# Kernel optimization log

Measured on AMD Instinct MI355X. Metric: run time of the kernel, lower is better.

## Reference

```python
import jax, jax.numpy as jnp
import numpy as np

EPS = 1e-3  # keras BatchNormalization default epsilon
K = 16


def _graph_feature(x, k):
    # x: [B, N, C] -> edge: [B, N, k, 2C]
    sq = jnp.sum(x * x, axis=-1)                       # [B, N]
    # negative squared distance (larger = closer); self is max
    pd = 2.0 * jnp.einsum('bnc,bmc->bnm', x, x) - sq[:, :, None] - sq[:, None, :]
    _, idx = jax.lax.top_k(pd, k)                      # [B, N, k]
    nbr = jax.vmap(lambda xb, ib: xb[ib])(x, idx)      # [B, N, k, C]
    ctr = jnp.broadcast_to(x[:, :, None, :], nbr.shape)
    return jnp.concatenate([ctr, nbr], axis=-1)        # [B, N, k, 2C]


def _bn(y, g, b, m, v):
    return (y - m) * (g * jax.lax.rsqrt(v + EPS)) + b


def _edge_block(x, W, g, b, m, v, k):
    e = _graph_feature(x, k)                           # [B, N, k, 2C]
    h = jnp.einsum('bnkc,cd->bnkd', e, W)              # 1x1 conv, no bias
    h = jax.nn.relu(_bn(h, g, b, m, v))
    return jnp.max(h, axis=2)                          # [B, N, D]


def setup_inputs() -> dict:
    key = jax.random.key(0)
    ks = jax.random.split(key, 32)
    B, N = 8, 2048
    x = jax.random.normal(ks[0], (B, N, 3), dtype=jnp.float32)
    dims = [(6, 64), (128, 64), (128, 128), (256, 256), (512, 512)]
    d = {'x': x}
    for i, (cin, cout) in enumerate(dims):
        j = i + 1
        d[f'W{j}'] = jax.random.normal(ks[1 + i], (cin, cout), dtype=jnp.float32) * (1.0 / np.sqrt(cin))
        d[f'g{j}'] = jax.random.uniform(ks[6 + i], (cout,), dtype=jnp.float32, minval=0.5, maxval=1.5)
        d[f'b{j}'] = jax.random.normal(ks[11 + i], (cout,), dtype=jnp.float32) * 0.1
        d[f'm{j}'] = jax.random.normal(ks[16 + i], (cout,), dtype=jnp.float32) * 0.1
        d[f'v{j}'] = jax.random.uniform(ks[21 + i], (cout,), dtype=jnp.float32, minval=0.5, maxval=1.5)
    return d


def reference(x, W1, g1, b1, m1, v1, W2, g2, b2, m2, v2, W3, g3, b3, m3, v3,
              W4, g4, b4, m4, v4, W5, g5, b5, m5, v5):
    x1 = _edge_block(x,  W1, g1, b1, m1, v1, K)   # [B, N, 64]
    x2 = _edge_block(x1, W2, g2, b2, m2, v2, K)   # [B, N, 64]
    x3 = _edge_block(x2, W3, g3, b3, m3, v3, K)   # [B, N, 128]
    x4 = _edge_block(x3, W4, g4, b4, m4, v4, K)   # [B, N, 256]
    x5 = jnp.concatenate([x1, x2, x3, x4], axis=-1)  # [B, N, 512]
    h5 = jnp.einsum('bnc,cd->bnd', x5, W5)           # 1x1 conv1d, no bias
    return jax.nn.relu(_bn(h5, g5, b5, m5, v5))      # [B, N, 512]
```

## Files before the change

kernel.cpp:

```cpp
#include <hip/hip_runtime.h>

#define NP 2048
#define BTOT 8
#define BN_TOT 16384
#define KC 16
#define NTILE 32
#define NEG_INF (-__builtin_inff())

typedef __attribute__((ext_vector_type(8))) short short8;
typedef __attribute__((ext_vector_type(4))) float f32x4;

__device__ __forceinline__ unsigned short bf16_rne(float x) {
  unsigned u = __float_as_uint(x);
  u += 0x7FFFu + ((u >> 16) & 1u);
  return (unsigned short)(u >> 16);
}
__device__ __forceinline__ void split2(float x, unsigned short& h, unsigned short& l) {
  h = bf16_rne(x);
  float hf = __uint_as_float((unsigned)h << 16);
  l = bf16_rne(x - hf);
}

__global__ __launch_bounds__(256) void dist_gemm(const float* __restrict__ X, int lda, int K,
                                                 const float* __restrict__ sq,
                                                 float* __restrict__ pd, int batch0) {
  int bz = blockIdx.z;
  const float* Xb = X + (size_t)(batch0 + bz) * NP * lda;
  const float* sqb = sq + (size_t)(batch0 + bz) * NP;
  float* pdb = pd + (size_t)bz * NP * NP;
  int rem = blockIdx.x, bi = 0;
  while (rem >= NTILE - bi) { rem -= NTILE - bi; ++bi; }
  int bj = bi + rem;
  int i0 = bi * 64, j0 = bj * 64;
  __shared__ float At[KC][68];
  __shared__ float Bt[KC][68];
  int t = threadIdx.x;
  int tx = t & 15, ty = t >> 4;
  int lk = t & 15, lr = t >> 4;
  float acc[4][4] = {};
  for (int k0 = 0; k0 < K; k0 += KC) {
    int kk = k0 + lk;
    bool kv = kk < K;
#pragma unroll
    for (int u = 0; u < 4; ++u) {
      int r = lr + u * 16;
      At[lk][r] = kv ? Xb[(size_t)(i0 + r) * lda + kk] : 0.f;
      Bt[lk][r] = kv ? Xb[(size_t)(j0 + r) * lda + kk] : 0.f;
    }
    __syncthreads();
#pragma unroll
    for (int q = 0; q < KC; ++q) {
      float4 a4 = *(const float4*)&At[q][ty * 4];
      float4 b4 = *(const float4*)&Bt[q][tx * 4];
      float a[4] = {a4.x, a4.y, a4.z, a4.w};
      float bv[4] = {b4.x, b4.y, b4.z, b4.w};
#pragma unroll
      for (int ii = 0; ii < 4; ++ii)
#pragma unroll
        for (int jj = 0; jj < 4; ++jj)
          acc[ii][jj] = fmaf(a[ii], bv[jj], acc[ii][jj]);
    }
    __syncthreads();
  }
  float4 sqj4 = *(const float4*)&sqb[j0 + tx * 4];
#pragma unroll
  for (int ii = 0; ii < 4; ++ii) {
    int i = i0 + ty * 4 + ii;
    float4 o;
    o.x = 2.f * acc[ii][0] - sqj4.x;
    o.y = 2.f * acc[ii][1] - sqj4.y;
    o.z = 2.f * acc[ii][2] - sqj4.z;
    o.w = 2.f * acc[ii][3] - sqj4.w;
    *(float4*)&pdb[(size_t)i * NP + j0 + tx * 4] = o;
  }
  if (bi != bj) {
    float4 sqi4 = *(const float4*)&sqb[i0 + ty * 4];
#pragma unroll
    for (int jj = 0; jj < 4; ++jj) {
      int j = j0 + tx * 4 + jj;
      float4 o;
      o.x = 2.f * acc[0][jj] - sqi4.x;
      o.y = 2.f * acc[1][jj] - sqi4.y;
      o.z = 2.f * acc[2][jj] - sqi4.z;
      o.w = 2.f * acc[3][jj] - sqi4.w;
      *(float4*)&pdb[(size_t)j * NP + i0 + ty * 4] = o;
    }
  }
}

template <typename JM>
__device__ __forceinline__ void select16(const float (&v)[32], int lane, float* svw,
                                         int* sjw, int* out, int jb, JM jmap) {
  float lmax = v[0];
#pragma unroll
  for (int t = 1; t < 32; ++t) lmax = fmaxf(lmax, v[t]);
  int rank = 0;
  for (int s = 0; s < 64; ++s) {
    float o = __shfl(lmax, s, 64);
    rank += (o > lmax) || (o == lmax && s < lane);
  }
  unsigned long long m15 = __ballot(rank == 15);
  float T0 = __shfl(lmax, (int)__builtin_ctzll(m15), 64);

  unsigned long long lowmask = (1ull << lane) - 1ull;
  unsigned keepmask = 0u;
  int base = 0;
#pragma unroll
  for (int t = 0; t < 32; ++t) {
    bool keep = (v[t] >= T0);
    unsigned long long mk = __ballot(keep);
    if (keep) {
      keepmask |= (1u << t);
      int pos = base + (int)__popcll(mk & lowmask);
      if (pos < 256) { svw[pos] = v[t]; sjw[pos] = jmap(t); }
    }
    base += (int)__popcll(mk);
  }
  int cnt = base;

  if (cnt <= 64) {
    __threadfence_block();
    float mv = NEG_INF;
    int mj = 1 << 30;
    if (lane < cnt) { mv = svw[lane]; mj = sjw[lane]; }
    int rk = 0;
    for (int s = 0; s < 64; ++s) {
      float ov = __shfl(mv, s, 64);
      int oj = __shfl(mj, s, 64);
      rk += (ov > mv) || (ov == mv && oj < mj);
    }
    if (lane < cnt && rk < 16) out[rk] = jb + mj;
    return;
  }

  if (cnt <= 256) {
    __threadfence_block();
    for (int r = 0; r < 16; ++r) {
      float lbv = NEG_INF;
      int lbj = 1 << 30, lbp = -1;
      for (int i = lane; i < cnt; i += 64) {
        float cv = svw[i];
        int cj = sjw[i];
        if (cv > lbv || (cv == lbv && cj < lbj)) { lbv = cv; lbj = cj; lbp = i; }
      }
      float bv = lbv;
      int bj = lbj;
#pragma unroll
      for (int off = 32; off > 0; off >>= 1) {
        float ov = __shfl_xor(bv, off, 64);
        int oj = __shfl_xor(bj, off, 64);
        if (ov > bv || (ov == bv && oj < bj)) { bv = ov; bj = oj; }
      }
      if (lane == 0) out[r] = jb + bj;
      if (lbp >= 0 && lbj == bj) svw[lbp] = NEG_INF;
      __threadfence_block();
    }
    return;
  }

  {
    unsigned avail = keepmask;
    for (int r = 0; r < 16; ++r) {
      float bv = NEG_INF;
      int bj = 1 << 30, bt = -1;
      unsigned am = avail;
      while (am) {
        int t = __builtin_ctz(am);
        am &= am - 1;
        float vv = v[t];
        int jj = jmap(t);
        if (vv > bv || (vv == bv && jj < bj)) { bv = vv; bj = jj; bt = t; }
      }
      float gv = bv;
      int gj = bj;
#pragma unroll
      for (int off = 32; off > 0; off >>= 1) {
        float ov = __shfl_xor(gv, off, 64);
        int oj = __shfl_xor(gj, off, 64);
        if (ov > gv || (ov == gv && oj < gj)) { gv = ov; gj = oj; }
      }
      if (lane == 0) out[r] = jb + gj;
      if (bt >= 0 && bj == gj) avail &= ~(1u << bt);
    }
  }
}

__global__ __launch_bounds__(256) void topk_kernel(const float* __restrict__ pd,
                                                   int* __restrict__ idx_out, int batch0) {
  __shared__ float sv[4][256];
  __shared__ int sj[4][256];
  int wave = threadIdx.x >> 6, lane = threadIdx.x & 63;
  int row = blockIdx.x * 4 + wave;
  const float* prow = pd + (size_t)row * NP;
  int grow = batch0 * NP + row;
  int jb = (grow >> 11) << 11;
  float v[32];
#pragma unroll
  for (int u = 0; u < 8; ++u) {
    float4 q = *(const float4*)&prow[u * 256 + (lane << 2)];
    v[u * 4 + 0] = q.x;
    v[u * 4 + 1] = q.y;
    v[u * 4 + 2] = q.z;
    v[u * 4 + 3] = q.w;
  }
  select16(v, lane, sv[wave], sj[wave], idx_out + (size_t)grow * 16, jb,
           [lane](int t) { return ((t >> 2) << 8) + (lane << 2) + (t & 3); });
}

__global__ __launch_bounds__(256) void dist3_topk(const float* __restrict__ x,
                                                  int* __restrict__ idx_out) {
  __shared__ float4 xs4[NP];
  __shared__ float sv[4][256];
  __shared__ int sj[4][256];
  int wave = threadIdx.x >> 6, lane = threadIdx.x & 63;
  int b = blockIdx.x >> 7;
  int row0 = (blockIdx.x & 127) * 16;
  const float* xb = x + (size_t)b * NP * 3;
  for (int n = threadIdx.x; n < NP; n += 256) {
    float a0 = xb[3 * n], a1 = xb[3 * n + 1], a2 = xb[3 * n + 2];
    xs4[n] = make_float4(a0, a1, a2, a0 * a0 + a1 * a1 + a2 * a2);
  }
  __syncthreads();
  int jb = b << 11;
  for (int rr = 0; rr < 4; ++rr) {
    int row = row0 + wave * 4 + rr;
    float4 c = xs4[row];
    float v[32];
#pragma unroll
    for (int t = 0; t < 32; ++t) {
      int j = lane + t * 64;
      float4 p = xs4[j];
      float dot = c.x * p.x + c.y * p.y + c.z * p.z;
      v[t] = 2.f * dot - p.w;
    }
    select16(v, lane, sv[wave], sj[wave], idx_out + (size_t)(jb + row) * 16, jb,
             [lane](int t) { return lane + t * 64; });
  }
}

__global__ __launch_bounds__(256) void feat_gemm(const float* __restrict__ A, int lda, int K,
                                                 const float* __restrict__ W, int D,
                                                 float* __restrict__ outT,
                                                 float* __restrict__ outB) {
  const float* Wz = W + (size_t)blockIdx.z * K * D;
  float* o = blockIdx.z ? outB : outT;
  int n0 = blockIdx.x * 64, m0 = blockIdx.y * 64;
  __shared__ float At[KC][68];
  __shared__ float Bt[KC][68];
  int t = threadIdx.x;
  int tx = t & 15, ty = t >> 4;
  float acc[4][4] = {};
  for (int k0 = 0; k0 < K; k0 += KC) {
    {
      int lk = t & 15, lr = t >> 4;
      int kk = k0 + lk;
      bool kv = kk < K;
#pragma unroll
      for (int u = 0; u < 4; ++u) {
        int r = lr + u * 16;
        At[lk][r] = kv ? A[(size_t)(m0 + r) * lda + kk] : 0.f;
      }
      int n = t & 63, kq0 = t >> 6;
#pragma unroll
      for (int u = 0; u < 4; ++u) {
        int kq = kq0 + u * 4;
        int kg = k0 + kq;
        Bt[kq][n] = (kg < K) ? Wz[(size_t)kg * D + n0 + n] : 0.f;
      }
    }
    __syncthreads();
#pragma unroll
    for (int q = 0; q < KC; ++q) {
      float4 a4 = *(const float4*)&At[q][ty * 4];
      float4 b4 = *(const float4*)&Bt[q][tx * 4];
      float a[4] = {a4.x, a4.y, a4.z, a4.w};
      float bv[4] = {b4.x, b4.y, b4.z, b4.w};
#pragma unroll
      for (int ii = 0; ii < 4; ++ii)
#pragma unroll
        for (int jj = 0; jj < 4; ++jj)
          acc[ii][jj] = fmaf(a[ii], bv[jj], acc[ii][jj]);
    }
    __syncthreads();
  }
#pragma unroll
  for (int ii = 0; ii < 4; ++ii) {
    float4 o4 = make_float4(acc[ii][0], acc[ii][1], acc[ii][2], acc[ii][3]);
    *(float4*)&o[(size_t)(m0 + ty * 4 + ii) * D + n0 + tx * 4] = o4;
  }
}

__global__ __launch_bounds__(256) void gather_bn_relu(const float* __restrict__ ZT,
                                                      const float* __restrict__ YB,
                                                      const int* __restrict__ idx, int D,
                                                      const float* __restrict__ g,
                                                      const float* __restrict__ bta,
                                                      const float* __restrict__ mu,
                                                      const float* __restrict__ va,
                                                      float* __restrict__ X5,
                                                      unsigned short* __restrict__ X5h,
                                                      unsigned short* __restrict__ X5l,
                                                      float* __restrict__ sqout, int coff) {
  __shared__ int nb[16];
  __shared__ float red[256];
  int bn = blockIdx.x, d = threadIdx.x;
  if (d < 16) nb[d] = idx[(size_t)bn * 16 + d];
  __syncthreads();
  float mx = NEG_INF;
#pragma unroll
  for (int j = 0; j < 16; ++j) mx = fmaxf(mx, YB[(size_t)nb[j] * D + d]);
  float h = ZT[(size_t)bn * D + d] + mx;
  float s = g[d] / sqrtf(va[d] + 1e-3f);
  float val = fmaxf((h - mu[d]) * s + bta[d], 0.f);
  size_t oi = (size_t)bn * 512 + coff + d;
  X5[oi] = val;
  unsigned short vh, vl;
  split2(val, vh, vl);
  X5h[oi] = vh;
  X5l[oi] = vl;
  red[d] = val * val;
  __syncthreads();
  for (int st = blockDim.x >> 1; st > 0; st >>= 1) {
    if (d < st) red[d] += red[d + st];
    __syncthreads();
  }
  if (d == 0) sqout[bn] = red[0];
}

__global__ __launch_bounds__(256) void w5t_split(const float* __restrict__ W5,
                                                 unsigned short* __restrict__ Wh,
                                                 unsigned short* __restrict__ Wl) {
  int n = blockIdx.x;
  for (int k = threadIdx.x; k < 512; k += 256) {
    unsigned short h, l;
    split2(W5[(size_t)k * 512 + n], h, l);
    Wh[(size_t)n * 512 + k] = h;
    Wl[(size_t)n * 512 + k] = l;
  }
}

__global__ __launch_bounds__(256) void final_mfma(const unsigned short* __restrict__ Ah,
                                                  const unsigned short* __restrict__ Al,
                                                  const unsigned short* __restrict__ Bh,
                                                  const unsigned short* __restrict__ Bl,
                                                  const float* __restrict__ g,
                                                  const float* __restrict__ bta,
                                                  const float* __restrict__ mu,
                                                  const float* __restrict__ va,
                                                  float* __restrict__ out) {
  int tid = threadIdx.x;
  int wave = tid >> 6, lane = tid & 63;
  int wm = wave >> 1, wn = wave & 1;
  int ln = lane & 15, quad = lane >> 4;
  int m_base = blockIdx.y * 128 + wm * 64;
  int n_base = blockIdx.x * 128 + wn * 64;

  f32x4 acc[4][4];
#pragma unroll
  for (int i = 0; i < 4; ++i)
#pragma unroll
    for (int j = 0; j < 4; ++j) acc[i][j] = (f32x4){0.f, 0.f, 0.f, 0.f};

  size_t aoff[4], boff[4];
#pragma unroll
  for (int t = 0; t < 4; ++t) {
    aoff[t] = (size_t)(m_base + t * 16 + ln) * 512 + quad * 8;
    boff[t] = (size_t)(n_base + t * 16 + ln) * 512 + quad * 8;
  }

  short8 cAh[4], cAl[4], cBh[4], cBl[4];
#pragma unroll
  for (int t = 0; t < 4; ++t) {
    cAh[t] = *(const short8*)(Ah + aoff[t]);
    cAl[t] = *(const short8*)(Al + aoff[t]);
    cBh[t] = *(const short8*)(Bh + boff[t]);
    cBl[t] = *(const short8*)(Bl + boff[t]);
  }

  for (int kk = 0; kk < 16; ++kk) {
    short8 nAh[4], nAl[4], nBh[4], nBl[4];
    if (kk < 15) {
      int ko = (kk + 1) * 32;
#pragma unroll
      for (int t = 0; t < 4; ++t) {
        nAh[t] = *(const short8*)(Ah + aoff[t] + ko);
        nAl[t] = *(const short8*)(Al + aoff[t] + ko);
        nBh[t] = *(const short8*)(Bh + boff[t] + ko);
        nBl[t] = *(const short8*)(Bl + boff[t] + ko);
      }
    }
#pragma unroll
    for (int tm = 0; tm < 4; ++tm)
#pragma unroll
      for (int tn = 0; tn < 4; ++tn) {
        acc[tm][tn] = __builtin_amdgcn_mfma_f32_16x16x32_bf16(cAh[tm], cBh[tn],
                                                              acc[tm][tn], 0, 0, 0);
        acc[tm][tn] = __builtin_amdgcn_mfma_f32_16x16x32_bf16(cAh[tm], cBl[tn],
                                                              acc[tm][tn], 0, 0, 0);
        acc[tm][tn] = __builtin_amdgcn_mfma_f32_16x16x32_bf16(cAl[tm], cBh[tn],
                                                              acc[tm][tn], 0, 0, 0);
      }
    if (kk < 15) {
#pragma unroll
      for (int t = 0; t < 4; ++t) {
        cAh[t] = nAh[t];
        cAl[t] = nAl[t];
        cBh[t] = nBh[t];
        cBl[t] = nBl[t];
      }
    }
  }

#pragma unroll
  for (int tn = 0; tn < 4; ++tn) {
    int col = n_base + tn * 16 + ln;
    float s = g[col] / sqrtf(va[col] + 1e-3f);
    float tc = bta[col] - mu[col] * s;
#pragma unroll
    for (int tm = 0; tm < 4; ++tm) {
      int mrow = m_base + tm * 16 + quad * 4;
#pragma unroll
      for (int r = 0; r < 4; ++r) {
        float val = acc[tm][tn][r] * s + tc;
        out[(size_t)(mrow + r) * 512 + col] = fmaxf(val, 0.f);
      }
    }
  }
}

extern "C" void kernel_launch(void* const* d_in, const int* in_sizes, int n_in,
                              void* d_out, int out_size, void* d_ws, size_t ws_size,
                              hipStream_t stream) {
  const float* x = (const float*)d_in[0];
  const float *W[5], *g[5], *bt[5], *mu[5], *va[5];
  for (int j = 0; j < 5; ++j) {
    W[j] = (const float*)d_in[1 + j * 5 + 0];
    g[j] = (const float*)d_in[1 + j * 5 + 1];
    bt[j] = (const float*)d_in[1 + j * 5 + 2];
    mu[j] = (const float*)d_in[1 + j * 5 + 3];
    va[j] = (const float*)d_in[1 + j * 5 + 4];
  }
  char* p = (char*)d_ws;
  float* X5 = (float*)p; p += (size_t)BN_TOT * 512 * 4;
  float* ZT = (float*)p; p += (size_t)BN_TOT * 256 * 4;
  float* YB = (float*)p; p += (size_t)BN_TOT * 256 * 4;
  int* idx = (int*)p;    p += (size_t)BN_TOT * 16 * 4;
  float* sq = (float*)p; p += (size_t)BN_TOT * 4;
  unsigned short* X5h = (unsigned short*)p; p += (size_t)BN_TOT * 512 * 2;
  unsigned short* X5l = (unsigned short*)p; p += (size_t)BN_TOT * 512 * 2;
  unsigned short* W5h = (unsigned short*)p; p += (size_t)512 * 512 * 2;
  unsigned short* W5l = (unsigned short*)p; p += (size_t)512 * 512 * 2;
  float* pd = (float*)p;
  size_t used = (size_t)(p - (char*)d_ws);
  size_t pdcap = (ws_size > used) ? (ws_size - used) / ((size_t)NP * NP * 4) : 0;
  int nb = (int)(pdcap < 1 ? 1 : (pdcap > (size_t)BTOT ? (size_t)BTOT : pdcap));

  w5t_split<<<512, 256, 0, stream>>>(W[4], W5h, W5l);

  struct Blk { const float* A; int lda, C, D, coff, w; };
  Blk blks[4] = {
      {x, 3, 3, 64, 0, 0},
      {X5 + 0, 512, 64, 64, 64, 1},
      {X5 + 64, 512, 64, 128, 128, 2},
      {X5 + 128, 512, 128, 256, 256, 3},
  };
  for (int q = 0; q < 4; ++q) {
    Blk& B = blks[q];
    if (q == 0) {
      dist3_topk<<<1024, 256, 0, stream>>>(x, idx);
    } else {
      for (int b0 = 0; b0 < BTOT; b0 += nb) {
        int cnt = (BTOT - b0 < nb) ? (BTOT - b0) : nb;
        dist_gemm<<<dim3(NTILE * (NTILE + 1) / 2, 1, cnt), 256, 0, stream>>>(
            B.A, B.lda, B.C, sq, pd, b0);
        topk_kernel<<<cnt * NP / 4, 256, 0, stream>>>(pd, idx, b0);
      }
    }
    feat_gemm<<<dim3(B.D / 64, BN_TOT / 64, 2), 256, 0, stream>>>(
        B.A, B.lda, B.C, W[B.w], B.D, ZT, YB);
    gather_bn_relu<<<BN_TOT, B.D, 0, stream>>>(ZT, YB, idx, B.D, g[B.w], bt[B.w], mu[B.w],
                                               va[B.w], X5, X5h, X5l, sq, B.coff);
  }
  final_mfma<<<dim3(4, 128), 256, 0, stream>>>(X5h, X5l, W5h, W5l, g[4], bt[4], mu[4],
                                               va[4], (float*)d_out);
}
```

Before: 623.8 us.

## Prune top-k candidates using per-16-column group maxima emitted by distance GEMM

The distance GEMM now also writes, for each row, the maximum over each 16-column group into a side buffer. The top-k kernel ranks these 128 group maxima, takes the 16th largest as a threshold, and reads only the groups at or above it from the distance matrix. The surviving candidates are then selected by a small rank or iterative argmax, and the kernel falls back to the full-row path when too many groups or candidates survive. This cuts the full 2048-wide row reads and selection work per row, at the cost of extra shuffles and stores in the GEMM epilogue and a larger workspace that may shrink how many batches fit per pass.

```diff
diff --git a/kernel.cpp b/kernel.cpp
--- a/kernel.cpp
+++ b/kernel.cpp
@@ -23,11 +23,13 @@
 
 __global__ __launch_bounds__(256) void dist_gemm(const float* __restrict__ X, int lda, int K,
                                                  const float* __restrict__ sq,
-                                                 float* __restrict__ pd, int batch0) {
+                                                 float* __restrict__ pd,
+                                                 float* __restrict__ gmax, int batch0) {
   int bz = blockIdx.z;
   const float* Xb = X + (size_t)(batch0 + bz) * NP * lda;
   const float* sqb = sq + (size_t)(batch0 + bz) * NP;
   float* pdb = pd + (size_t)bz * NP * NP;
+  float* gmb = gmax + (size_t)bz * NP * 128;
   int rem = blockIdx.x, bi = 0;
   while (rem >= NTILE - bi) { rem -= NTILE - bi; ++bi; }
   int bj = bi + rem;
@@ -35,7 +37,7 @@
   __shared__ float At[KC][68];
   __shared__ float Bt[KC][68];
   int t = threadIdx.x;
-  int tx = t & 15, ty = t >> 4;
+  int tx = t & 15, ty = t >> 4, wv = t >> 6;
   int lk = t & 15, lr = t >> 4;
   float acc[4][4] = {};
   for (int k0 = 0; k0 < K; k0 += KC) {
@@ -63,6 +65,7 @@
     __syncthreads();
   }
   float4 sqj4 = *(const float4*)&sqb[j0 + tx * 4];
+  float gmI[4];
 #pragma unroll
   for (int ii = 0; ii < 4; ++ii) {
     int i = i0 + ty * 4 + ii;
@@ -72,18 +75,42 @@
     o.z = 2.f * acc[ii][2] - sqj4.z;
     o.w = 2.f * acc[ii][3] - sqj4.w;
     *(float4*)&pdb[(size_t)i * NP + j0 + tx * 4] = o;
+    gmI[ii] = fmaxf(fmaxf(o.x, o.y), fmaxf(o.z, o.w));
+  }
+#pragma unroll
+  for (int ii = 0; ii < 4; ++ii) {
+    gmI[ii] = fmaxf(gmI[ii], __shfl_xor(gmI[ii], 1, 64));
+    gmI[ii] = fmaxf(gmI[ii], __shfl_xor(gmI[ii], 2, 64));
+  }
+  if ((tx & 3) == 0) {
+#pragma unroll
+    for (int ii = 0; ii < 4; ++ii)
+      gmb[(size_t)(i0 + ty * 4 + ii) * 128 + bj * 4 + (tx >> 2)] = gmI[ii];
   }
   if (bi != bj) {
     float4 sqi4 = *(const float4*)&sqb[i0 + ty * 4];
+    float sqi[4] = {sqi4.x, sqi4.y, sqi4.z, sqi4.w};
+    float gmJ[4];
 #pragma unroll
     for (int jj = 0; jj < 4; ++jj) {
       int j = j0 + tx * 4 + jj;
       float4 o;
-      o.x = 2.f * acc[0][jj] - sqi4.x;
-      o.y = 2.f * acc[1][jj] - sqi4.y;
-      o.z = 2.f * acc[2][jj] - sqi4.z;
-      o.w = 2.f * acc[3][jj] - sqi4.w;
+      o.x = 2.f * acc[0][jj] - sqi[0];
+      o.y = 2.f * acc[1][jj] - sqi[1];
+      o.z = 2.f * acc[2][jj] - sqi[2];
+      o.w = 2.f * acc[3][jj] - sqi[3];
       *(float4*)&pdb[(size_t)j * NP + i0 + ty * 4] = o;
+      gmJ[jj] = fmaxf(fmaxf(o.x, o.y), fmaxf(o.z, o.w));
+    }
+#pragma unroll
+    for (int jj = 0; jj < 4; ++jj) {
+      gmJ[jj] = fmaxf(gmJ[jj], __shfl_xor(gmJ[jj], 16, 64));
+      gmJ[jj] = fmaxf(gmJ[jj], __shfl_xor(gmJ[jj], 32, 64));
+    }
+    if ((t & 63) < 16) {
+#pragma unroll
+      for (int jj = 0; jj < 4; ++jj)
+        gmb[(size_t)(j0 + tx * 4 + jj) * 128 + bi * 4 + wv] = gmJ[jj];
     }
   }
 }
@@ -185,15 +212,8 @@
   }
 }
 
-__global__ __launch_bounds__(256) void topk_kernel(const float* __restrict__ pd,
-                                                   int* __restrict__ idx_out, int batch0) {
-  __shared__ float sv[4][256];
-  __shared__ int sj[4][256];
-  int wave = threadIdx.x >> 6, lane = threadIdx.x & 63;
-  int row = blockIdx.x * 4 + wave;
-  const float* prow = pd + (size_t)row * NP;
-  int grow = batch0 * NP + row;
-  int jb = (grow >> 11) << 11;
+__device__ __forceinline__ void topk_full_row(const float* __restrict__ prow, int lane,
+                                              float* svw, int* sjw, int* out, int jb) {
   float v[32];
 #pragma unroll
   for (int u = 0; u < 8; ++u) {
@@ -203,8 +223,117 @@
     v[u * 4 + 2] = q.z;
     v[u * 4 + 3] = q.w;
   }
-  select16(v, lane, sv[wave], sj[wave], idx_out + (size_t)grow * 16, jb,
+  select16(v, lane, svw, sjw, out, jb,
            [lane](int t) { return ((t >> 2) << 8) + (lane << 2) + (t & 3); });
+}
+
+__global__ __launch_bounds__(256) void topk_kernel(const float* __restrict__ pd,
+                                                   const float* __restrict__ gmax,
+                                                   int* __restrict__ idx_out, int batch0) {
+  __shared__ float sv[4][256];
+  __shared__ int sj[4][256];
+  __shared__ int gl[4][128];
+  int wave = threadIdx.x >> 6, lane = threadIdx.x & 63;
+  int row = blockIdx.x * 4 + wave;
+  const float* prow = pd + (size_t)row * NP;
+  const float* gmr = gmax + (size_t)row * 128;
+  int grow = batch0 * NP + row;
+  int jb = (grow >> 11) << 11;
+  int* out = idx_out + (size_t)grow * 16;
+
+  float gm0 = gmr[lane], gm1 = gmr[lane + 64];
+  int r0 = 0, r1 = 0;
+  for (int s = 0; s < 64; ++s) {
+    float o0 = __shfl(gm0, s, 64);
+    float o1 = __shfl(gm1, s, 64);
+    r0 += (o0 > gm0) || (o0 == gm0 && s < lane);
+    r0 += (o1 > gm0);
+    r1 += (o0 >= gm1);
+    r1 += (o1 > gm1) || (o1 == gm1 && s < lane);
+  }
+  float G16;
+  unsigned long long b0 = __ballot(r0 == 15);
+  if (b0)
+    G16 = __shfl(gm0, (int)__builtin_ctzll(b0), 64);
+  else {
+    unsigned long long b1 = __ballot(r1 == 15);
+    G16 = __shfl(gm1, (int)__builtin_ctzll(b1), 64);
+  }
+
+  unsigned long long lowmask = (1ull << lane) - 1ull;
+  unsigned long long k0 = __ballot(gm0 >= G16);
+  unsigned long long k1 = __ballot(gm1 >= G16);
+  int c0 = (int)__popcll(k0);
+  if (gm0 >= G16) gl[wave][(int)__popcll(k0 & lowmask)] = lane;
+  if (gm1 >= G16) gl[wave][c0 + (int)__popcll(k1 & lowmask)] = lane + 64;
+  int gcnt = c0 + (int)__popcll(k1);
+  __threadfence_block();
+
+  if (gcnt > 32) {
+    topk_full_row(prow, lane, sv[wave], sj[wave], out, jb);
+    return;
+  }
+
+  int cnt = 0;
+  for (int bg = 0; bg < gcnt; bg += 16) {
+    int gi = bg + (lane >> 2);
+    bool act = gi < gcnt;
+    int g = act ? gl[wave][gi] : 0;
+    float4 q = *(const float4*)&prow[g * 16 + (lane & 3) * 4];
+    float qa[4] = {q.x, q.y, q.z, q.w};
+#pragma unroll
+    for (int t = 0; t < 4; ++t) {
+      bool keep = act && (qa[t] >= G16);
+      unsigned long long mk = __ballot(keep);
+      if (keep) {
+        int pos = cnt + (int)__popcll(mk & lowmask);
+        if (pos < 256) {
+          sv[wave][pos] = qa[t];
+          sj[wave][pos] = g * 16 + (lane & 3) * 4 + t;
+        }
+      }
+      cnt += (int)__popcll(mk);
+    }
+  }
+  if (cnt > 256) {
+    topk_full_row(prow, lane, sv[wave], sj[wave], out, jb);
+    return;
+  }
+  __threadfence_block();
+
+  if (cnt <= 64) {
+    float mv = NEG_INF;
+    int mj = 1 << 30;
+    if (lane < cnt) { mv = sv[wave][lane]; mj = sj[wave][lane]; }
+    int rk = 0;
+    for (int s = 0; s < 64; ++s) {
+      float ov = __shfl(mv, s, 64);
+      int oj = __shfl(mj, s, 64);
+      rk += (ov > mv) || (ov == mv && oj < mj);
+    }
+    if (lane < cnt && rk < 16) out[rk] = jb + mj;
+    return;
+  }
+  for (int r = 0; r < 16; ++r) {
+    float lbv = NEG_INF;
+    int lbj = 1 << 30, lbp = -1;
+    for (int i = lane; i < cnt; i += 64) {
+      float cv = sv[wave][i];
+      int cj = sj[wave][i];
+      if (cv > lbv || (cv == lbv && cj < lbj)) { lbv = cv; lbj = cj; lbp = i; }
+    }
+    float bv = lbv;
+    int bj = lbj;
+#pragma unroll
+    for (int off = 32; off > 0; off >>= 1) {
+      float ov = __shfl_xor(bv, off, 64);
+      int oj = __shfl_xor(bj, off, 64);
+      if (ov > bv || (ov == bv && oj < bj)) { bv = ov; bj = oj; }
+    }
+    if (lane == 0) out[r] = jb + bj;
+    if (lbp >= 0 && lbj == bj) sv[wave][lbp] = NEG_INF;
+    __threadfence_block();
+  }
 }
 
 __global__ __launch_bounds__(256) void dist3_topk(const float* __restrict__ x,
@@ -450,6 +579,7 @@
   unsigned short* X5l = (unsigned short*)p; p += (size_t)BN_TOT * 512 * 2;
   unsigned short* W5h = (unsigned short*)p; p += (size_t)512 * 512 * 2;
   unsigned short* W5l = (unsigned short*)p; p += (size_t)512 * 512 * 2;
+  float* gmax = (float*)p; p += (size_t)BTOT * NP * 128 * 4;
   float* pd = (float*)p;
   size_t used = (size_t)(p - (char*)d_ws);
   size_t pdcap = (ws_size > used) ? (ws_size - used) / ((size_t)NP * NP * 4) : 0;
@@ -472,8 +602,8 @@
       for (int b0 = 0; b0 < BTOT; b0 += nb) {
         int cnt = (BTOT - b0 < nb) ? (BTOT - b0) : nb;
         dist_gemm<<<dim3(NTILE * (NTILE + 1) / 2, 1, cnt), 256, 0, stream>>>(
-            B.A, B.lda, B.C, sq, pd, b0);
-        topk_kernel<<<cnt * NP / 4, 256, 0, stream>>>(pd, idx, b0);
+            B.A, B.lda, B.C, sq, pd, gmax, b0);
+        topk_kernel<<<cnt * NP / 4, 256, 0, stream>>>(pd, gmax, idx, b0);
       }
     }
     feat_gemm<<<dim3(B.D / 64, BN_TOT / 64, 2), 256, 0, stream>>>(
```

Result: slower. 655.0 us (+5.0%).
